# Optimization experiments

Measured on AMD Instinct MI355X. Metric: run time of the kernel, lower is better.

## Reference

```python
import jax, jax.numpy as jnp
import numpy as np
import math

B, N, D, K, H = 64, 16384, 64, 8, 128
ITERS = 3
LN_EPS = 1e-5  # torch LayerNorm default


def _ln(x, w, b):
    m = jnp.mean(x, axis=-1, keepdims=True)
    v = jnp.mean((x - m) ** 2, axis=-1, keepdims=True)
    return (x - m) * jax.lax.rsqrt(v + LN_EPS) * w + b


def setup_inputs() -> dict:
    key = jax.random.key(0)
    ks = jax.random.split(key, 20)
    s = 1.0 / math.sqrt(D)
    inp = {
        "inputs": jax.random.normal(ks[0], (B, N, D), jnp.float32),
        "noise": jax.random.normal(ks[1], (B, K, D), jnp.float32),
        "slots_mu": jax.random.normal(ks[2], (1, 1, D), jnp.float32),
        "slots_sigma": jax.random.uniform(ks[3], (1, 1, D), jnp.float32, -s, s),
        "ln_in_w": jnp.ones((D,), jnp.float32), "ln_in_b": jnp.zeros((D,), jnp.float32),
        "ln_slots_w": jnp.ones((D,), jnp.float32), "ln_slots_b": jnp.zeros((D,), jnp.float32),
        "ln_ff_w": jnp.ones((D,), jnp.float32), "ln_ff_b": jnp.zeros((D,), jnp.float32),
        "wk": jax.random.uniform(ks[4], (D, D), jnp.float32, -s, s),
        "bk": jax.random.uniform(ks[5], (D,), jnp.float32, -s, s),
        "wq": jax.random.uniform(ks[6], (D, D), jnp.float32, -s, s),
        "bq": jax.random.uniform(ks[7], (D,), jnp.float32, -s, s),
        "wv": jax.random.uniform(ks[8], (D, D), jnp.float32, -s, s),
        "bv": jax.random.uniform(ks[9], (D,), jnp.float32, -s, s),
        "gru_wih": jax.random.uniform(ks[10], (D, 3 * D), jnp.float32, -s, s),
        "gru_bih": jax.random.uniform(ks[11], (3 * D,), jnp.float32, -s, s),
        "gru_whh": jax.random.uniform(ks[12], (D, 3 * D), jnp.float32, -s, s),
        "gru_bhh": jax.random.uniform(ks[13], (3 * D,), jnp.float32, -s, s),
        "mlp_w1": jax.random.uniform(ks[14], (D, H), jnp.float32, -s, s),
        "mlp_b1": jax.random.uniform(ks[15], (H,), jnp.float32, -s, s),
        "mlp_w2": jax.random.uniform(ks[16], (H, D), jnp.float32, -1.0 / math.sqrt(H), 1.0 / math.sqrt(H)),
        "mlp_b2": jax.random.uniform(ks[17], (D,), jnp.float32, -1.0 / math.sqrt(H), 1.0 / math.sqrt(H)),
    }
    return inp


def reference(inputs, noise, slots_mu, slots_sigma, ln_in_w, ln_in_b,
              ln_slots_w, ln_slots_b, ln_ff_w, ln_ff_b,
              wk, bk, wq, bq, wv, bv,
              gru_wih, gru_bih, gru_whh, gru_bhh,
              mlp_w1, mlp_b1, mlp_w2, mlp_b2):
    x = _ln(inputs, ln_in_w, ln_in_b)              # [B, N, D]
    # k, v depend only on (fixed) inputs; original recomputes them each iter
    # with identical values, so hoist for efficiency (same math).
    k = x @ wk + bk                                 # [B, N, D]
    v = x @ wv + bv                                 # [B, N, D]
    slots = slots_mu + slots_sigma * noise          # [B, K, D]
    scale = 1.0 / math.sqrt(D)
    for _ in range(ITERS):
        prev = slots
        q = _ln(slots, ln_slots_w, ln_slots_b) @ wq + bq          # [B, K, D]
        logits = jnp.einsum('bkd,bnd->bkn', q, k) * scale          # [B, K, N]
        attn = jax.nn.softmax(logits, axis=1)  # softmax over slots
        updates = jnp.einsum('bkn,bnd->bkd', attn, v)              # [B, K, D]
        # torch GRUCell: gates ordered (r, z, n)
        gi = updates @ gru_wih + gru_bih                           # [B, K, 3D]
        gh = prev @ gru_whh + gru_bhh
        i_r, i_z, i_n = jnp.split(gi, 3, axis=-1)
        h_r, h_z, h_n = jnp.split(gh, 3, axis=-1)
        r = jax.nn.sigmoid(i_r + h_r)
        z = jax.nn.sigmoid(i_z + h_z)
        n = jnp.tanh(i_n + r * h_n)
        slots = (1.0 - z) * n + z * prev
        h = _ln(slots, ln_ff_w, ln_ff_b)
        slots = slots + (jax.nn.relu(h @ mlp_w1 + mlp_b1) @ mlp_w2 + mlp_b2)
    return slots
```

## Files before the change

kernel.cpp:

```cpp
#include <hip/hip_runtime.h>
#include <math.h>

#define B_ 64
#define N_ 16384
#define D_ 64
#define K_ 8
#define SCALE 0.125f
#define LN_EPS 1e-5f
#define CHUNKS 8
#define ROWS_PER_CHUNK (N_ / CHUNKS)
#define TILES (ROWS_PER_CHUNK / 256)
#define REC 528

__device__ __forceinline__ float wsum64(float v) {
#pragma unroll
  for (int m = 1; m < 64; m <<= 1) v += __shfl_xor(v, m);
  return v;
}

__global__ void init_slots(const float* __restrict__ noise, const float* __restrict__ mu,
                           const float* __restrict__ sg, float* __restrict__ slots) {
  int i = blockIdx.x * blockDim.x + threadIdx.x;
  int d = i & 63;
  slots[i] = mu[d] + sg[d] * noise[i];
}

__global__ __launch_bounds__(64) void prep_q(
    const float* __restrict__ slots,
    const float* __restrict__ lnsw, const float* __restrict__ lnsb,
    const float* __restrict__ wq, const float* __restrict__ bq,
    const float* __restrict__ wk, const float* __restrict__ bk,
    const float* __restrict__ lniw, const float* __restrict__ lnib,
    float* __restrict__ qprep) {
  const int bk_i = blockIdx.x;
  const int b = bk_i >> 3, kk = bk_i & 7;
  const int d = threadIdx.x;
  __shared__ float xs[64], qsh[64], wkl[64 * 65];
  for (int i = 0; i < 64; ++i) wkl[i * 65 + d] = wk[i * 64 + d];
  float s = slots[bk_i * 64 + d];
  float m = wsum64(s) * (1.f / 64.f);
  float df = s - m;
  float var = wsum64(df * df) * (1.f / 64.f);
  float r = 1.f / sqrtf(var + LN_EPS);
  xs[d] = df * r * lnsw[d] + lnsb[d];
  __syncthreads();
  float q = bq[d];
  for (int c = 0; c < 64; ++c) q += xs[c] * wq[c * 64 + d];
  qsh[d] = q;
  __syncthreads();
  float qp = 0.f, c0 = 0.f;
  for (int dd = 0; dd < 64; ++dd) {
    float qd = qsh[dd];
    qp += wkl[d * 65 + dd] * qd;
    c0 += qd * bk[dd];
  }
  float qw = qp * lniw[d] * SCALE;
  float As = wsum64(qw);
  float Bp = wsum64(qp * lnib[d]);
  float Bc = (Bp + c0) * SCALE;
  float* rec = qprep + b * REC;
  rec[d * 8 + kk] = qw;
  if (d == 0) { rec[512 + kk] = As; rec[520 + kk] = Bc; }
}

__global__ __launch_bounds__(256, 2) void attn_pass(
    const float* __restrict__ inp, const float* __restrict__ qprep,
    float* __restrict__ part) {
  __shared__ __align__(16) float xrow[256 * 68];
  __shared__ float2 aw[4 * 257];
  __shared__ float redST[64];
  const int tid = threadIdx.x;
  const int b = blockIdx.x >> 3, chunk = blockIdx.x & 7;
  const int p = tid & 3, dq = (tid >> 2) & 15, w = tid >> 6;
  const float* __restrict__ qp = qprep + b * REC;
  const float* srcbase = inp + ((size_t)b * N_ + (size_t)chunk * ROWS_PER_CHUNK) * D_;
  float4 x[16];
  {
    const float4* s = reinterpret_cast<const float4*>(srcbase + (size_t)tid * D_);
#pragma unroll
    for (int j = 0; j < 16; ++j) x[j] = s[j];
  }
  float Ya[8] = {0.f, 0.f, 0.f, 0.f, 0.f, 0.f, 0.f, 0.f};
  float sS[8] = {0.f, 0.f, 0.f, 0.f, 0.f, 0.f, 0.f, 0.f};
  float sT[8] = {0.f, 0.f, 0.f, 0.f, 0.f, 0.f, 0.f, 0.f};
  for (int t = 0; t < TILES; ++t) {
    float sum = 0.f, sq = 0.f;
    float l[8] = {0.f, 0.f, 0.f, 0.f, 0.f, 0.f, 0.f, 0.f};
#pragma unroll
    for (int j = 0; j < 16; ++j) {
      float xc[4] = {x[j].x, x[j].y, x[j].z, x[j].w};
#pragma unroll
      for (int e = 0; e < 4; ++e) {
        const int c = j * 4 + e;
        const float v = xc[e];
        sum += v; sq += v * v;
#pragma unroll
        for (int kq = 0; kq < 8; ++kq) l[kq] += qp[c * 8 + kq] * v;
      }
    }
    const float m = sum * (1.f / 64.f);
    const float var = sq * (1.f / 64.f) - m * m;
    const float r = 1.f / sqrtf(var + LN_EPS);
    const float mr = m * r;
    float lmax = -1e30f;
#pragma unroll
    for (int kq = 0; kq < 8; ++kq) {
      l[kq] = r * l[kq] - mr * qp[512 + kq] + qp[520 + kq];
      lmax = fmaxf(lmax, l[kq]);
    }
    float es = 0.f;
#pragma unroll
    for (int kq = 0; kq < 8; ++kq) { l[kq] = __expf(l[kq] - lmax); es += l[kq]; }
    const float inv = 1.f / es;
#pragma unroll
    for (int kq = 0; kq < 8; ++kq) {
      l[kq] *= inv;
      sS[kq] += l[kq];
      sT[kq] += l[kq] * mr;
    }
#pragma unroll
    for (int pp = 0; pp < 4; ++pp) {
      float2 v2; v2.x = l[2 * pp] * r; v2.y = l[2 * pp + 1] * r;
      aw[pp * 257 + tid] = v2;
    }
    {
      float* dst = &xrow[tid * 68];
      const int rs = tid >> 3;
#pragma unroll
      for (int j = 0; j < 16; ++j) {
        const int cs = (j + rs) & 15;
        *reinterpret_cast<float4*>(dst + cs * 4) = x[j];
      }
    }
    if (t + 1 < TILES) {
      const float4* s = reinterpret_cast<const float4*>(srcbase + (size_t)((t + 1) * 256 + tid) * D_);
#pragma unroll
      for (int j = 0; j < 16; ++j) x[j] = s[j];
    }
    __syncthreads();
#pragma unroll 4
    for (int i = 0; i < 64; ++i) {
      const int nl = w * 64 + i;
      const float2 a2 = aw[p * 257 + nl];
      const float4 xv = *reinterpret_cast<const float4*>(
          &xrow[nl * 68 + (((dq + (nl >> 3)) & 15) << 2)]);
      Ya[0] += a2.x * xv.x; Ya[1] += a2.x * xv.y; Ya[2] += a2.x * xv.z; Ya[3] += a2.x * xv.w;
      Ya[4] += a2.y * xv.x; Ya[5] += a2.y * xv.y; Ya[6] += a2.y * xv.z; Ya[7] += a2.y * xv.w;
    }
    __syncthreads();
  }
#pragma unroll
  for (int kq = 0; kq < 8; ++kq) { sS[kq] = wsum64(sS[kq]); sT[kq] = wsum64(sT[kq]); }
  if ((tid & 63) == 0) {
#pragma unroll
    for (int i = 0; i < 8; ++i) { redST[w * 16 + i] = sS[i]; redST[w * 16 + 8 + i] = sT[i]; }
  }
  float* yred = xrow;
  *reinterpret_cast<float4*>(&yred[tid * 12]) = make_float4(Ya[0], Ya[1], Ya[2], Ya[3]);
  *reinterpret_cast<float4*>(&yred[tid * 12 + 4]) = make_float4(Ya[4], Ya[5], Ya[6], Ya[7]);
  __syncthreads();
  float* dst = part + (size_t)blockIdx.x * REC;
  for (int o = tid; o < 512; o += 256) {
    const int kq = o >> 6, dd = o & 63;
    const int pp = kq >> 1, kkl = kq & 1, dqq = dd >> 2, jj = dd & 3;
    float v = 0.f;
#pragma unroll
    for (int ww = 0; ww < 4; ++ww)
      v += yred[(ww * 64 + dqq * 4 + pp) * 12 + kkl * 4 + jj];
    dst[o] = v;
  }
  if (tid < 16)
    dst[512 + tid] = redST[tid] + redST[16 + tid] + redST[32 + tid] + redST[48 + tid];
}

__global__ __launch_bounds__(256) void slot_update(
    const float* __restrict__ part, const float* slots_in,
    const float* __restrict__ lniw, const float* __restrict__ lnib,
    const float* __restrict__ wv, const float* __restrict__ bv,
    const float* __restrict__ wih, const float* __restrict__ bih,
    const float* __restrict__ whh, const float* __restrict__ bhh,
    const float* __restrict__ lnfw, const float* __restrict__ lnfb,
    const float* __restrict__ w1, const float* __restrict__ b1,
    const float* __restrict__ w2, const float* __restrict__ b2,
    const float* __restrict__ lnsw, const float* __restrict__ lnsb,
    const float* __restrict__ wq, const float* __restrict__ bq,
    const float* __restrict__ wk, const float* __restrict__ bkv,
    float* slots_out, float* __restrict__ qprep, const int do_prep) {
  const int bk_i = blockIdx.x, b = bk_i >> 3, kk = bk_i & 7;
  const int tid = threadIdx.x, cq = tid >> 6, d = tid & 63;
  const int c0 = cq * 16;
  __shared__ float pA[4][68], pB[4][68], pC[4][68], pD[4][68];
  __shared__ float xsh[64], psh[64], ush[64], hsh[64], snsh[64], qsh[64];
  __shared__ float hid1[2][132];
  const float* pb = part + (size_t)(b * CHUNKS) * REC;
  float S = 0.f, T1 = 0.f;
#pragma unroll
  for (int ch = 0; ch < CHUNKS; ++ch) {
    S += pb[ch * REC + 512 + kk];
    T1 += pb[ch * REC + 520 + kk];
  }
  float y = 0.f;
#pragma unroll
  for (int cc = 0; cc < 2; ++cc)
    y += pb[(cq * 2 + cc) * REC + kk * 64 + d];
  pA[cq][d] = y;
  const float prev = slots_in[bk_i * 64 + d];
  if (cq == 0) psh[d] = prev;
  __syncthreads();
  if (cq == 0) {
    const float Y = pA[0][d] + pA[1][d] + pA[2][d] + pA[3][d];
    xsh[d] = lniw[d] * (Y - T1) + lnib[d] * S;
  }
  __syncthreads();
  {
    float up = 0.f, h0 = 0.f, h1 = 0.f, h2 = 0.f;
    for (int c = c0; c < c0 + 16; ++c) {
      const float xc = xsh[c], pc = psh[c];
      up += wv[c * 64 + d] * xc;
      h0 += pc * whh[c * 192 + d];
      h1 += pc * whh[c * 192 + 64 + d];
      h2 += pc * whh[c * 192 + 128 + d];
    }
    pA[cq][d] = up; pB[cq][d] = h0; pC[cq][d] = h1; pD[cq][d] = h2;
  }
  __syncthreads();
  float hh0 = 0.f, hh1 = 0.f, hh2 = 0.f;
  if (cq == 0) {
    ush[d] = S * bv[d] + pA[0][d] + pA[1][d] + pA[2][d] + pA[3][d];
    hh0 = bhh[d] + pB[0][d] + pB[1][d] + pB[2][d] + pB[3][d];
    hh1 = bhh[64 + d] + pC[0][d] + pC[1][d] + pC[2][d] + pC[3][d];
    hh2 = bhh[128 + d] + pD[0][d] + pD[1][d] + pD[2][d] + pD[3][d];
  }
  __syncthreads();
  {
    float g0 = 0.f, g1 = 0.f, g2 = 0.f;
    for (int c = c0; c < c0 + 16; ++c) {
      const float uc = ush[c];
      g0 += uc * wih[c * 192 + d];
      g1 += uc * wih[c * 192 + 64 + d];
      g2 += uc * wih[c * 192 + 128 + d];
    }
    pA[cq][d] = g0; pB[cq][d] = g1; pC[cq][d] = g2;
  }
  __syncthreads();
  if (cq == 0) {
    const float gi0 = bih[d] + pA[0][d] + pA[1][d] + pA[2][d] + pA[3][d];
    const float gi1 = bih[64 + d] + pB[0][d] + pB[1][d] + pB[2][d] + pB[3][d];
    const float gi2 = bih[128 + d] + pC[0][d] + pC[1][d] + pC[2][d] + pC[3][d];
    const float rg = 1.f / (1.f + __expf(-(gi0 + hh0)));
    const float zg = 1.f / (1.f + __expf(-(gi1 + hh1)));
    const float ng = tanhf(gi2 + rg * hh2);
    const float sn = (1.f - zg) * ng + zg * prev;
    const float mm = wsum64(sn) * (1.f / 64.f);
    const float df = sn - mm;
    const float vv = wsum64(df * df) * (1.f / 64.f);
    const float rr = 1.f / sqrtf(vv + LN_EPS);
    snsh[d] = sn;
    hsh[d] = df * rr * lnfw[d] + lnfb[d];
  }
  __syncthreads();
  {
    const int j = tid & 127, ch2 = tid >> 7;
    float a = 0.f;
    for (int c = ch2 * 32; c < ch2 * 32 + 32; ++c) a += hsh[c] * w1[c * 128 + j];
    hid1[ch2][j] = a;
  }
  __syncthreads();
  {
    float o = 0.f;
    for (int j2 = cq * 32; j2 < cq * 32 + 32; ++j2) {
      const float hv = fmaxf(hid1[0][j2] + hid1[1][j2] + b1[j2], 0.f);
      o += hv * w2[j2 * 64 + d];
    }
    pA[cq][d] = o;
  }
  __syncthreads();
  float news = 0.f;
  if (cq == 0) {
    news = snsh[d] + b2[d] + pA[0][d] + pA[1][d] + pA[2][d] + pA[3][d];
    slots_out[bk_i * 64 + d] = news;
  }
  if (!do_prep) return;
  if (cq == 0) {
    const float mm = wsum64(news) * (1.f / 64.f);
    const float df = news - mm;
    const float vv = wsum64(df * df) * (1.f / 64.f);
    const float rr = 1.f / sqrtf(vv + LN_EPS);
    xsh[d] = df * rr * lnsw[d] + lnsb[d];
  }
  __syncthreads();
  {
    float qpt = 0.f;
    for (int c = c0; c < c0 + 16; ++c) qpt += xsh[c] * wq[c * 64 + d];
    pB[cq][d] = qpt;
  }
  __syncthreads();
  if (cq == 0) qsh[d] = bq[d] + pB[0][d] + pB[1][d] + pB[2][d] + pB[3][d];
  __syncthreads();
  {
    float qq = 0.f;
    for (int dd2 = c0; dd2 < c0 + 16; ++dd2) qq += wk[d * 64 + dd2] * qsh[dd2];
    pC[cq][d] = qq;
  }
  __syncthreads();
  if (cq == 0) {
    const float qpv = pC[0][d] + pC[1][d] + pC[2][d] + pC[3][d];
    const float c0v = wsum64(qsh[d] * bkv[d]);
    const float qw = qpv * lniw[d] * SCALE;
    const float As = wsum64(qw);
    const float Bp = wsum64(qpv * lnib[d]);
    const float Bc = (Bp + c0v) * SCALE;
    float* rec = qprep + b * REC;
    rec[d * 8 + kk] = qw;
    if (d == 0) { rec[512 + kk] = As; rec[520 + kk] = Bc; }
  }
}

extern "C" void kernel_launch(void* const* d_in, const int* in_sizes, int n_in,
                              void* d_out, int out_size, void* d_ws, size_t ws_size,
                              hipStream_t stream) {
  const float* inp   = (const float*)d_in[0];
  const float* noise = (const float*)d_in[1];
  const float* mu    = (const float*)d_in[2];
  const float* sg    = (const float*)d_in[3];
  const float* lniw  = (const float*)d_in[4];
  const float* lnib  = (const float*)d_in[5];
  const float* lnsw  = (const float*)d_in[6];
  const float* lnsb  = (const float*)d_in[7];
  const float* lnfw  = (const float*)d_in[8];
  const float* lnfb  = (const float*)d_in[9];
  const float* wk    = (const float*)d_in[10];
  const float* bk    = (const float*)d_in[11];
  const float* wq    = (const float*)d_in[12];
  const float* bq    = (const float*)d_in[13];
  const float* wv    = (const float*)d_in[14];
  const float* bv    = (const float*)d_in[15];
  const float* wih   = (const float*)d_in[16];
  const float* bih   = (const float*)d_in[17];
  const float* whh   = (const float*)d_in[18];
  const float* bhh   = (const float*)d_in[19];
  const float* w1    = (const float*)d_in[20];
  const float* b1    = (const float*)d_in[21];
  const float* w2    = (const float*)d_in[22];
  const float* b2    = (const float*)d_in[23];
  float* ws = (float*)d_ws;
  float* slots = ws;
  float* qprep = ws + 32768;
  float* part  = ws + 32768 + 64 * REC;
  float* out   = (float*)d_out;
  init_slots<<<64, 512, 0, stream>>>(noise, mu, sg, slots);
  prep_q<<<B_ * K_, 64, 0, stream>>>(slots, lnsw, lnsb, wq, bq, wk, bk, lniw, lnib, qprep);
  for (int it = 0; it < 3; ++it) {
    attn_pass<<<B_ * CHUNKS, 256, 0, stream>>>(inp, qprep, part);
    slot_update<<<B_ * K_, 256, 0, stream>>>(
        part, slots, lniw, lnib, wv, bv, wih, bih, whh, bhh,
        lnfw, lnfb, w1, b1, w2, b2, lnsw, lnsb, wq, bq, wk, bk,
        (it == 2) ? out : slots, qprep, (it < 2) ? 1 : 0);
  }
}
```

Baseline: 376.2 us.

## Double-buffer attention input tiles via direct global-to-LDS DMA loads

Restructures attn_pass to stream input tiles straight into shared memory with global_load_lds into a double buffer, so the next tile's fetch overlaps compute on the current one. Blocks grow to 512 threads over fewer chunks, with two threads splitting each row's logit dot products and combining them by shuffle. Query weights are staged in LDS for vector reads. This is meant to cut register pressure and global load latency stalls, at the cost of hand-placed waitcnt and barrier synchronisation that must be exactly right. The S/T partial sums are halved because both threads of a pair add them.

Measured after the change: 318.4 us. 15.4% less time.

```diff
diff --git a/kernel.cpp b/kernel.cpp
--- a/kernel.cpp
+++ b/kernel.cpp
@@ -3,19 +3,25 @@
 
 #define B_ 64
 #define N_ 16384
-#define D_ 64
 #define K_ 8
 #define SCALE 0.125f
 #define LN_EPS 1e-5f
-#define CHUNKS 8
+#define CHUNKS 4
 #define ROWS_PER_CHUNK (N_ / CHUNKS)
-#define TILES (ROWS_PER_CHUNK / 256)
+#define TILE 256
+#define TILES (ROWS_PER_CHUNK / TILE)
 #define REC 528
 
 __device__ __forceinline__ float wsum64(float v) {
 #pragma unroll
   for (int m = 1; m < 64; m <<= 1) v += __shfl_xor(v, m);
   return v;
+}
+
+__device__ __forceinline__ void dma16(const float* g, float* l) {
+  __builtin_amdgcn_global_load_lds(
+      (const __attribute__((address_space(1))) float*)g,
+      (__attribute__((address_space(3))) float*)l, 16, 0, 0);
 }
 
 __global__ void init_slots(const float* __restrict__ noise, const float* __restrict__ mu,
@@ -63,41 +69,85 @@
   if (d == 0) { rec[512 + kk] = As; rec[520 + kk] = Bc; }
 }
 
-__global__ __launch_bounds__(256, 2) void attn_pass(
+__global__ __launch_bounds__(512, 2) void attn_pass(
     const float* __restrict__ inp, const float* __restrict__ qprep,
     float* __restrict__ part) {
-  __shared__ __align__(16) float xrow[256 * 68];
-  __shared__ float2 aw[4 * 257];
-  __shared__ float redST[64];
+  __shared__ __align__(16) float xbuf[2][TILE * 64];
+  __shared__ __align__(16) float qwT[512];
+  __shared__ float2 aw[4][TILE + 4];
+  __shared__ float redST[128];
   const int tid = threadIdx.x;
-  const int b = blockIdx.x >> 3, chunk = blockIdx.x & 7;
-  const int p = tid & 3, dq = (tid >> 2) & 15, w = tid >> 6;
+  const int b = blockIdx.x >> 2, chunk = blockIdx.x & 3;
+  const int w = tid >> 6;
   const float* __restrict__ qp = qprep + b * REC;
-  const float* srcbase = inp + ((size_t)b * N_ + (size_t)chunk * ROWS_PER_CHUNK) * D_;
-  float4 x[16];
-  {
-    const float4* s = reinterpret_cast<const float4*>(srcbase + (size_t)tid * D_);
-#pragma unroll
-    for (int j = 0; j < 16; ++j) x[j] = s[j];
-  }
-  float Ya[8] = {0.f, 0.f, 0.f, 0.f, 0.f, 0.f, 0.f, 0.f};
-  float sS[8] = {0.f, 0.f, 0.f, 0.f, 0.f, 0.f, 0.f, 0.f};
-  float sT[8] = {0.f, 0.f, 0.f, 0.f, 0.f, 0.f, 0.f, 0.f};
+  const float* srcbase = inp + ((size_t)b * N_ + (size_t)chunk * ROWS_PER_CHUNK) * 64;
+  qwT[tid] = qp[tid];
+  float As_[8], Bc_[8];
+#pragma unroll
+  for (int kq = 0; kq < 8; ++kq) { As_[kq] = qp[512 + kq]; Bc_[kq] = qp[520 + kq]; }
+  __syncthreads();
+  {
+    const float* tb = srcbase;
+    float* lb = &xbuf[0][0];
+#pragma unroll
+    for (int r8 = 0; r8 < 8; ++r8) {
+      const int R = r8 * 32 + (tid >> 4);
+      const int q = tid & 15;
+      const int lj = (q - R) & 15;
+      dma16(tb + R * 64 + lj * 4, lb + (r8 * 512 + (tid & ~63)) * 4);
+    }
+  }
+  const int h = tid & 1, R = tid >> 1;
+  const int p = (tid & 63) >> 4, dqv = tid & 15;
+  float Ya[8] = {0,0,0,0,0,0,0,0};
+  float sS[8] = {0,0,0,0,0,0,0,0};
+  float sT[8] = {0,0,0,0,0,0,0,0};
   for (int t = 0; t < TILES; ++t) {
+    const int cur = t & 1;
+    __builtin_amdgcn_s_barrier();
+    if (t + 1 < TILES) {
+      const float* tb = srcbase + (size_t)(t + 1) * TILE * 64;
+      float* lb = &xbuf[cur ^ 1][0];
+#pragma unroll
+      for (int r8 = 0; r8 < 8; ++r8) {
+        const int Rr = r8 * 32 + (tid >> 4);
+        const int q = tid & 15;
+        const int lj = (q - Rr) & 15;
+        dma16(tb + Rr * 64 + lj * 4, lb + (r8 * 512 + (tid & ~63)) * 4);
+      }
+      asm volatile("s_waitcnt vmcnt(8)" ::: "memory");
+    } else {
+      asm volatile("s_waitcnt vmcnt(0)" ::: "memory");
+    }
+    __builtin_amdgcn_sched_barrier(0);
+    __builtin_amdgcn_s_barrier();
+    const float* rowp = &xbuf[cur][R * 64];
+    float4 xq[8];
+#pragma unroll
+    for (int jj = 0; jj < 8; ++jj) {
+      const int qph = (h * 8 + jj + R) & 15;
+      xq[jj] = *reinterpret_cast<const float4*>(&rowp[qph * 4]);
+    }
     float sum = 0.f, sq = 0.f;
-    float l[8] = {0.f, 0.f, 0.f, 0.f, 0.f, 0.f, 0.f, 0.f};
-#pragma unroll
-    for (int j = 0; j < 16; ++j) {
-      float xc[4] = {x[j].x, x[j].y, x[j].z, x[j].w};
+    float l[8] = {0,0,0,0,0,0,0,0};
+#pragma unroll
+    for (int jj = 0; jj < 8; ++jj) {
+      float xc[4] = {xq[jj].x, xq[jj].y, xq[jj].z, xq[jj].w};
 #pragma unroll
       for (int e = 0; e < 4; ++e) {
-        const int c = j * 4 + e;
+        const int c = h * 32 + jj * 4 + e;
         const float v = xc[e];
         sum += v; sq += v * v;
-#pragma unroll
-        for (int kq = 0; kq < 8; ++kq) l[kq] += qp[c * 8 + kq] * v;
+        const float4 qa = *reinterpret_cast<const float4*>(&qwT[c * 8]);
+        const float4 qb = *reinterpret_cast<const float4*>(&qwT[c * 8 + 4]);
+        l[0] += qa.x * v; l[1] += qa.y * v; l[2] += qa.z * v; l[3] += qa.w * v;
+        l[4] += qb.x * v; l[5] += qb.y * v; l[6] += qb.z * v; l[7] += qb.w * v;
       }
     }
+#pragma unroll
+    for (int kq = 0; kq < 8; ++kq) l[kq] += __shfl_xor(l[kq], 1);
+    sum += __shfl_xor(sum, 1);
+    sq  += __shfl_xor(sq, 1);
     const float m = sum * (1.f / 64.f);
     const float var = sq * (1.f / 64.f) - m * m;
     const float r = 1.f / sqrtf(var + LN_EPS);
@@ -105,7 +155,7 @@
     float lmax = -1e30f;
 #pragma unroll
     for (int kq = 0; kq < 8; ++kq) {
-      l[kq] = r * l[kq] - mr * qp[512 + kq] + qp[520 + kq];
+      l[kq] = r * l[kq] - mr * As_[kq] + Bc_[kq];
       lmax = fmaxf(lmax, l[kq]);
     }
     float es = 0.f;
@@ -118,36 +168,24 @@
       sS[kq] += l[kq];
       sT[kq] += l[kq] * mr;
     }
-#pragma unroll
-    for (int pp = 0; pp < 4; ++pp) {
-      float2 v2; v2.x = l[2 * pp] * r; v2.y = l[2 * pp + 1] * r;
-      aw[pp * 257 + tid] = v2;
-    }
-    {
-      float* dst = &xrow[tid * 68];
-      const int rs = tid >> 3;
-#pragma unroll
-      for (int j = 0; j < 16; ++j) {
-        const int cs = (j + rs) & 15;
-        *reinterpret_cast<float4*>(dst + cs * 4) = x[j];
+    if (h == 0) {
+#pragma unroll
+      for (int pp = 0; pp < 4; ++pp) {
+        float2 v2; v2.x = l[2 * pp] * r; v2.y = l[2 * pp + 1] * r;
+        aw[pp][R] = v2;
       }
     }
-    if (t + 1 < TILES) {
-      const float4* s = reinterpret_cast<const float4*>(srcbase + (size_t)((t + 1) * 256 + tid) * D_);
-#pragma unroll
-      for (int j = 0; j < 16; ++j) x[j] = s[j];
-    }
-    __syncthreads();
-#pragma unroll 4
-    for (int i = 0; i < 64; ++i) {
-      const int nl = w * 64 + i;
-      const float2 a2 = aw[p * 257 + nl];
+    asm volatile("s_waitcnt lgkmcnt(0)" ::: "memory");
+    __builtin_amdgcn_s_barrier();
+#pragma unroll 8
+    for (int i = 0; i < 32; ++i) {
+      const int nl = w * 32 + i;
+      const float2 a2 = aw[p][nl];
       const float4 xv = *reinterpret_cast<const float4*>(
-          &xrow[nl * 68 + (((dq + (nl >> 3)) & 15) << 2)]);
+          &xbuf[cur][nl * 64 + (((dqv + nl) & 15) << 2)]);
       Ya[0] += a2.x * xv.x; Ya[1] += a2.x * xv.y; Ya[2] += a2.x * xv.z; Ya[3] += a2.x * xv.w;
       Ya[4] += a2.y * xv.x; Ya[5] += a2.y * xv.y; Ya[6] += a2.y * xv.z; Ya[7] += a2.y * xv.w;
     }
-    __syncthreads();
   }
 #pragma unroll
   for (int kq = 0; kq < 8; ++kq) { sS[kq] = wsum64(sS[kq]); sT[kq] = wsum64(sT[kq]); }
@@ -155,22 +193,24 @@
 #pragma unroll
     for (int i = 0; i < 8; ++i) { redST[w * 16 + i] = sS[i]; redST[w * 16 + 8 + i] = sT[i]; }
   }
-  float* yred = xrow;
-  *reinterpret_cast<float4*>(&yred[tid * 12]) = make_float4(Ya[0], Ya[1], Ya[2], Ya[3]);
-  *reinterpret_cast<float4*>(&yred[tid * 12 + 4]) = make_float4(Ya[4], Ya[5], Ya[6], Ya[7]);
-  __syncthreads();
+  float* yr = &xbuf[0][0];
+  *reinterpret_cast<float4*>(&yr[tid * 8])     = make_float4(Ya[0], Ya[1], Ya[2], Ya[3]);
+  *reinterpret_cast<float4*>(&yr[tid * 8 + 4]) = make_float4(Ya[4], Ya[5], Ya[6], Ya[7]);
+  asm volatile("s_waitcnt lgkmcnt(0)" ::: "memory");
+  __builtin_amdgcn_s_barrier();
   float* dst = part + (size_t)blockIdx.x * REC;
-  for (int o = tid; o < 512; o += 256) {
-    const int kq = o >> 6, dd = o & 63;
-    const int pp = kq >> 1, kkl = kq & 1, dqq = dd >> 2, jj = dd & 3;
+  {
+    const int kq = tid >> 6, dd = tid & 63;
+    const int pp = kq >> 1, cc = kq & 1, dqq = dd >> 2, ee = dd & 3;
     float v = 0.f;
 #pragma unroll
-    for (int ww = 0; ww < 4; ++ww)
-      v += yred[(ww * 64 + dqq * 4 + pp) * 12 + kkl * 4 + jj];
-    dst[o] = v;
+    for (int ww = 0; ww < 8; ++ww)
+      v += yr[(ww * 64 + pp * 16 + dqq) * 8 + cc * 4 + ee];
+    dst[tid] = v;
   }
   if (tid < 16)
-    dst[512 + tid] = redST[tid] + redST[16 + tid] + redST[32 + tid] + redST[48 + tid];
+    dst[512 + tid] = 0.5f * (redST[tid] + redST[16 + tid] + redST[32 + tid] + redST[48 + tid] +
+                             redST[64 + tid] + redST[80 + tid] + redST[96 + tid] + redST[112 + tid]);
 }
 
 __global__ __launch_bounds__(256) void slot_update(
@@ -199,11 +239,7 @@
     S += pb[ch * REC + 512 + kk];
     T1 += pb[ch * REC + 520 + kk];
   }
-  float y = 0.f;
-#pragma unroll
-  for (int cc = 0; cc < 2; ++cc)
-    y += pb[(cq * 2 + cc) * REC + kk * 64 + d];
-  pA[cq][d] = y;
+  pA[cq][d] = pb[cq * REC + kk * 64 + d];
   const float prev = slots_in[bk_i * 64 + d];
   if (cq == 0) psh[d] = prev;
   __syncthreads();
@@ -351,7 +387,7 @@
   init_slots<<<64, 512, 0, stream>>>(noise, mu, sg, slots);
   prep_q<<<B_ * K_, 64, 0, stream>>>(slots, lnsw, lnsb, wq, bq, wk, bk, lniw, lnib, qprep);
   for (int it = 0; it < 3; ++it) {
-    attn_pass<<<B_ * CHUNKS, 256, 0, stream>>>(inp, qprep, part);
+    attn_pass<<<B_ * CHUNKS, 512, 0, stream>>>(inp, qprep, part);
     slot_update<<<B_ * K_, 256, 0, stream>>>(
         part, slots, lniw, lnib, wv, bv, wih, bih, whh, bhh,
         lnfw, lnfb, w1, b1, w2, b2, lnsw, lnsb, wq, bq, wk, bk,
```

## Stream input tiles via async global-to-LDS double buffering in attention pass

Applied to the files above, without the earlier changes.

The attention kernel now loads input rows straight into a double-buffered LDS tile with global_load_lds instead of staging them through registers and writing them to shared memory. The next tile's transfer overlaps with compute on the current one, synchronised by explicit waitcnt counters and barriers. The weighted-sum loop is restructured so each thread accumulates all 8 slots for 4 columns across 16 rows. The chunk count per batch drops to 4, which halves the grid to 256 blocks and removes the register-heavy launch bound. The larger LDS footprint (about 143 KB) and the smaller grid lower occupancy and parallelism.

After: 414.5 us. 10.2% more time.

```diff
diff --git a/kernel.cpp b/kernel.cpp
--- a/kernel.cpp
+++ b/kernel.cpp
@@ -3,19 +3,26 @@
 
 #define B_ 64
 #define N_ 16384
-#define D_ 64
 #define K_ 8
 #define SCALE 0.125f
 #define LN_EPS 1e-5f
-#define CHUNKS 8
+#define CHUNKS 4
 #define ROWS_PER_CHUNK (N_ / CHUNKS)
-#define TILES (ROWS_PER_CHUNK / 256)
+#define TILE 256
+#define TILES (ROWS_PER_CHUNK / TILE)
+#define CHSTR 260
 #define REC 528
 
 __device__ __forceinline__ float wsum64(float v) {
 #pragma unroll
   for (int m = 1; m < 64; m <<= 1) v += __shfl_xor(v, m);
   return v;
+}
+
+__device__ __forceinline__ void dma16(const float* g, float* l) {
+  __builtin_amdgcn_global_load_lds(
+      (const __attribute__((address_space(1))) float*)g,
+      (__attribute__((address_space(3))) float*)l, 16, 0, 0);
 }
 
 __global__ void init_slots(const float* __restrict__ noise, const float* __restrict__ mu,
@@ -63,32 +70,61 @@
   if (d == 0) { rec[512 + kk] = As; rec[520 + kk] = Bc; }
 }
 
-__global__ __launch_bounds__(256, 2) void attn_pass(
+__global__ __launch_bounds__(256) void attn_pass(
     const float* __restrict__ inp, const float* __restrict__ qprep,
     float* __restrict__ part) {
-  __shared__ __align__(16) float xrow[256 * 68];
-  __shared__ float2 aw[4 * 257];
+  __shared__ __align__(16) float xbuf[2][64 * CHSTR];
+  __shared__ __align__(16) float awb[256 * 10];
   __shared__ float redST[64];
   const int tid = threadIdx.x;
-  const int b = blockIdx.x >> 3, chunk = blockIdx.x & 7;
-  const int p = tid & 3, dq = (tid >> 2) & 15, w = tid >> 6;
+  const int w = tid >> 6, lane = tid & 63;
+  const int b = blockIdx.x >> 2, chunk4 = blockIdx.x & 3;
   const float* __restrict__ qp = qprep + b * REC;
-  const float* srcbase = inp + ((size_t)b * N_ + (size_t)chunk * ROWS_PER_CHUNK) * D_;
-  float4 x[16];
-  {
-    const float4* s = reinterpret_cast<const float4*>(srcbase + (size_t)tid * D_);
-#pragma unroll
-    for (int j = 0; j < 16; ++j) x[j] = s[j];
-  }
-  float Ya[8] = {0.f, 0.f, 0.f, 0.f, 0.f, 0.f, 0.f, 0.f};
-  float sS[8] = {0.f, 0.f, 0.f, 0.f, 0.f, 0.f, 0.f, 0.f};
-  float sT[8] = {0.f, 0.f, 0.f, 0.f, 0.f, 0.f, 0.f, 0.f};
+  const float* srcbase = inp + ((size_t)b * N_ + (size_t)chunk4 * ROWS_PER_CHUNK) * 64;
+  float As_[8], Bc_[8];
+#pragma unroll
+  for (int kq = 0; kq < 8; ++kq) { As_[kq] = qp[512 + kq]; Bc_[kq] = qp[520 + kq]; }
+#pragma unroll
+  for (int i = 0; i < 16; ++i) {
+    const int ch = w * 16 + i;
+    dma16(srcbase + ch * 256 + lane * 4, &xbuf[0][ch * CHSTR]);
+  }
+  const int R = tid;
+  const int g = lane >> 4, q = lane & 15;
+  float Ya[8][4];
+  float sS[8], sT[8];
+#pragma unroll
+  for (int kq = 0; kq < 8; ++kq) {
+    sS[kq] = 0.f; sT[kq] = 0.f;
+#pragma unroll
+    for (int e = 0; e < 4; ++e) Ya[kq][e] = 0.f;
+  }
   for (int t = 0; t < TILES; ++t) {
+    const int cur = t & 1;
+    asm volatile("s_waitcnt lgkmcnt(0)" ::: "memory");
+    __builtin_amdgcn_s_barrier();
+    __builtin_amdgcn_sched_barrier(0);
+    if (t + 1 < TILES) {
+      const float* tb = srcbase + (size_t)(t + 1) * TILE * 64;
+      float* lb = &xbuf[cur ^ 1][0];
+#pragma unroll
+      for (int i = 0; i < 16; ++i) {
+        const int ch = w * 16 + i;
+        dma16(tb + ch * 256 + lane * 4, lb + ch * CHSTR);
+      }
+      asm volatile("s_waitcnt vmcnt(16)" ::: "memory");
+    } else {
+      asm volatile("s_waitcnt vmcnt(0)" ::: "memory");
+    }
+    __builtin_amdgcn_sched_barrier(0);
+    __builtin_amdgcn_s_barrier();
+    const float* rowp = &xbuf[cur][(R >> 2) * CHSTR + (R & 3) * 64];
     float sum = 0.f, sq = 0.f;
-    float l[8] = {0.f, 0.f, 0.f, 0.f, 0.f, 0.f, 0.f, 0.f};
+    float l[8] = {0, 0, 0, 0, 0, 0, 0, 0};
 #pragma unroll
     for (int j = 0; j < 16; ++j) {
-      float xc[4] = {x[j].x, x[j].y, x[j].z, x[j].w};
+      const float4 xv = *reinterpret_cast<const float4*>(rowp + j * 4);
+      const float xc[4] = {xv.x, xv.y, xv.z, xv.w};
 #pragma unroll
       for (int e = 0; e < 4; ++e) {
         const int c = j * 4 + e;
@@ -105,7 +141,7 @@
     float lmax = -1e30f;
 #pragma unroll
     for (int kq = 0; kq < 8; ++kq) {
-      l[kq] = r * l[kq] - mr * qp[512 + kq] + qp[520 + kq];
+      l[kq] = r * l[kq] - mr * As_[kq] + Bc_[kq];
       lmax = fmaxf(lmax, l[kq]);
     }
     float es = 0.f;
@@ -114,59 +150,52 @@
     const float inv = 1.f / es;
 #pragma unroll
     for (int kq = 0; kq < 8; ++kq) {
-      l[kq] *= inv;
-      sS[kq] += l[kq];
-      sT[kq] += l[kq] * mr;
-    }
-#pragma unroll
-    for (int pp = 0; pp < 4; ++pp) {
-      float2 v2; v2.x = l[2 * pp] * r; v2.y = l[2 * pp + 1] * r;
-      aw[pp * 257 + tid] = v2;
-    }
-    {
-      float* dst = &xrow[tid * 68];
-      const int rs = tid >> 3;
-#pragma unroll
-      for (int j = 0; j < 16; ++j) {
-        const int cs = (j + rs) & 15;
-        *reinterpret_cast<float4*>(dst + cs * 4) = x[j];
+      const float a = l[kq] * inv;
+      sS[kq] += a;
+      sT[kq] += a * mr;
+      l[kq] = a * r;
+    }
+    *reinterpret_cast<float4*>(&awb[R * 10])     = make_float4(l[0], l[1], l[2], l[3]);
+    *reinterpret_cast<float4*>(&awb[R * 10 + 4]) = make_float4(l[4], l[5], l[6], l[7]);
+    asm volatile("s_waitcnt lgkmcnt(0)" ::: "memory");
+    __builtin_amdgcn_s_barrier();
+#pragma unroll 4
+    for (int i = 0; i < 16; ++i) {
+      const int chb = w * 16 + i;
+      const float* ap = &awb[(chb * 4 + g) * 10];
+      const float4 a0 = *reinterpret_cast<const float4*>(ap);
+      const float4 a1 = *reinterpret_cast<const float4*>(ap + 4);
+      const float4 xv = *reinterpret_cast<const float4*>(
+          &xbuf[cur][chb * CHSTR + g * 64 + (q << 2)]);
+      const float xc[4] = {xv.x, xv.y, xv.z, xv.w};
+#pragma unroll
+      for (int e = 0; e < 4; ++e) {
+        Ya[0][e] += a0.x * xc[e]; Ya[1][e] += a0.y * xc[e];
+        Ya[2][e] += a0.z * xc[e]; Ya[3][e] += a0.w * xc[e];
+        Ya[4][e] += a1.x * xc[e]; Ya[5][e] += a1.y * xc[e];
+        Ya[6][e] += a1.z * xc[e]; Ya[7][e] += a1.w * xc[e];
       }
     }
-    if (t + 1 < TILES) {
-      const float4* s = reinterpret_cast<const float4*>(srcbase + (size_t)((t + 1) * 256 + tid) * D_);
-#pragma unroll
-      for (int j = 0; j < 16; ++j) x[j] = s[j];
-    }
-    __syncthreads();
-#pragma unroll 4
-    for (int i = 0; i < 64; ++i) {
-      const int nl = w * 64 + i;
-      const float2 a2 = aw[p * 257 + nl];
-      const float4 xv = *reinterpret_cast<const float4*>(
-          &xrow[nl * 68 + (((dq + (nl >> 3)) & 15) << 2)]);
-      Ya[0] += a2.x * xv.x; Ya[1] += a2.x * xv.y; Ya[2] += a2.x * xv.z; Ya[3] += a2.x * xv.w;
-      Ya[4] += a2.y * xv.x; Ya[5] += a2.y * xv.y; Ya[6] += a2.y * xv.z; Ya[7] += a2.y * xv.w;
-    }
-    __syncthreads();
   }
 #pragma unroll
   for (int kq = 0; kq < 8; ++kq) { sS[kq] = wsum64(sS[kq]); sT[kq] = wsum64(sT[kq]); }
-  if ((tid & 63) == 0) {
+  if (lane == 0) {
 #pragma unroll
     for (int i = 0; i < 8; ++i) { redST[w * 16 + i] = sS[i]; redST[w * 16 + 8 + i] = sT[i]; }
   }
-  float* yred = xrow;
-  *reinterpret_cast<float4*>(&yred[tid * 12]) = make_float4(Ya[0], Ya[1], Ya[2], Ya[3]);
-  *reinterpret_cast<float4*>(&yred[tid * 12 + 4]) = make_float4(Ya[4], Ya[5], Ya[6], Ya[7]);
+  float* yr = &xbuf[0][0];
+#pragma unroll
+  for (int kq = 0; kq < 8; ++kq)
+    *reinterpret_cast<float4*>(yr + tid * 36 + kq * 4) =
+        make_float4(Ya[kq][0], Ya[kq][1], Ya[kq][2], Ya[kq][3]);
   __syncthreads();
   float* dst = part + (size_t)blockIdx.x * REC;
   for (int o = tid; o < 512; o += 256) {
-    const int kq = o >> 6, dd = o & 63;
-    const int pp = kq >> 1, kkl = kq & 1, dqq = dd >> 2, jj = dd & 3;
+    const int kq = o >> 6, col = o & 63;
+    const int qq = col >> 2, ee = col & 3;
     float v = 0.f;
 #pragma unroll
-    for (int ww = 0; ww < 4; ++ww)
-      v += yred[(ww * 64 + dqq * 4 + pp) * 12 + kkl * 4 + jj];
+    for (int s = 0; s < 16; ++s) v += yr[(s * 16 + qq) * 36 + kq * 4 + ee];
     dst[o] = v;
   }
   if (tid < 16)
@@ -199,11 +228,7 @@
     S += pb[ch * REC + 512 + kk];
     T1 += pb[ch * REC + 520 + kk];
   }
-  float y = 0.f;
-#pragma unroll
-  for (int cc = 0; cc < 2; ++cc)
-    y += pb[(cq * 2 + cc) * REC + kk * 64 + d];
-  pA[cq][d] = y;
+  pA[cq][d] = pb[cq * REC + kk * 64 + d];
   const float prev = slots_in[bk_i * 64 + d];
   if (cq == 0) psh[d] = prev;
   __syncthreads();
```

## Restructure attention pass into per-wave fp16 LDS tiles with more chunks

Applied to the files above, without the earlier changes.

The attention pass now gives each wave its own 64-row tile, staged in LDS as packed fp16 pairs together with fp16 attention weights. This removes the block-wide __syncthreads between the logit and accumulation phases and halves LDS footprint so four blocks fit per CU. The chunk count doubles to 16 per batch, and slot_update sums the extra partials. Storing x and attention weights in fp16 adds rounding error in the updates accumulation, and the register prefetch of the next tile is dropped.

Measured after the change: 319.3 us. 15.1% less time.

```diff
diff --git a/kernel.cpp b/kernel.cpp
--- a/kernel.cpp
+++ b/kernel.cpp
@@ -3,19 +3,28 @@
 
 #define B_ 64
 #define N_ 16384
-#define D_ 64
 #define K_ 8
 #define SCALE 0.125f
 #define LN_EPS 1e-5f
-#define CHUNKS 8
-#define ROWS_PER_CHUNK (N_ / CHUNKS)
-#define TILES (ROWS_PER_CHUNK / 256)
+#define CHUNKS 16
 #define REC 528
+
+typedef unsigned int u32;
+typedef __fp16 half2_t __attribute__((ext_vector_type(2)));
 
 __device__ __forceinline__ float wsum64(float v) {
 #pragma unroll
   for (int m = 1; m < 64; m <<= 1) v += __shfl_xor(v, m);
   return v;
+}
+
+__device__ __forceinline__ u32 pk16(float a, float b) {
+  half2_t h = __builtin_amdgcn_cvt_pkrtz(a, b);
+  return __builtin_bit_cast(u32, h);
+}
+__device__ __forceinline__ float2 up16(u32 u) {
+  half2_t h = __builtin_bit_cast(half2_t, u);
+  return make_float2((float)h.x, (float)h.y);
 }
 
 __global__ void init_slots(const float* __restrict__ noise, const float* __restrict__ mu,
@@ -63,32 +72,35 @@
   if (d == 0) { rec[512 + kk] = As; rec[520 + kk] = Bc; }
 }
 
-__global__ __launch_bounds__(256, 2) void attn_pass(
+__global__ __launch_bounds__(256, 4) void attn_pass(
     const float* __restrict__ inp, const float* __restrict__ qprep,
     float* __restrict__ part) {
-  __shared__ __align__(16) float xrow[256 * 68];
-  __shared__ float2 aw[4 * 257];
+  __shared__ u32 xls[4][64 * 34];
+  __shared__ u32 awl[4][64 * 5];
   __shared__ float redST[64];
   const int tid = threadIdx.x;
-  const int b = blockIdx.x >> 3, chunk = blockIdx.x & 7;
-  const int p = tid & 3, dq = (tid >> 2) & 15, w = tid >> 6;
+  const int w = tid >> 6, lane = tid & 63;
+  const int b = blockIdx.x >> 4, chunk = blockIdx.x & 15;
   const float* __restrict__ qp = qprep + b * REC;
-  const float* srcbase = inp + ((size_t)b * N_ + (size_t)chunk * ROWS_PER_CHUNK) * D_;
-  float4 x[16];
-  {
-    const float4* s = reinterpret_cast<const float4*>(srcbase + (size_t)tid * D_);
-#pragma unroll
-    for (int j = 0; j < 16; ++j) x[j] = s[j];
-  }
-  float Ya[8] = {0.f, 0.f, 0.f, 0.f, 0.f, 0.f, 0.f, 0.f};
-  float sS[8] = {0.f, 0.f, 0.f, 0.f, 0.f, 0.f, 0.f, 0.f};
-  float sT[8] = {0.f, 0.f, 0.f, 0.f, 0.f, 0.f, 0.f, 0.f};
-  for (int t = 0; t < TILES; ++t) {
+  const float* srcw = inp + ((size_t)b * N_ + (size_t)(chunk * 1024 + w * 256)) * 64;
+  float As_[8], Bc_[8];
+#pragma unroll
+  for (int kq = 0; kq < 8; ++kq) { As_[kq] = qp[512 + kq]; Bc_[kq] = qp[520 + kq]; }
+  u32* __restrict__ xw = xls[w];
+  u32* __restrict__ aww = awl[w];
+  const int rh = lane >> 5, kh = (lane >> 3) & 3, c8 = lane & 7;
+  float Y0[8] = {0, 0, 0, 0, 0, 0, 0, 0};
+  float Y1[8] = {0, 0, 0, 0, 0, 0, 0, 0};
+  float sS[8] = {0, 0, 0, 0, 0, 0, 0, 0};
+  float sT[8] = {0, 0, 0, 0, 0, 0, 0, 0};
+  for (int mt = 0; mt < 4; ++mt) {
+    const float4* src = reinterpret_cast<const float4*>(srcw + (size_t)(mt * 64 + lane) * 64);
     float sum = 0.f, sq = 0.f;
-    float l[8] = {0.f, 0.f, 0.f, 0.f, 0.f, 0.f, 0.f, 0.f};
+    float l[8] = {0, 0, 0, 0, 0, 0, 0, 0};
 #pragma unroll
     for (int j = 0; j < 16; ++j) {
-      float xc[4] = {x[j].x, x[j].y, x[j].z, x[j].w};
+      const float4 xv = src[j];
+      const float xc[4] = {xv.x, xv.y, xv.z, xv.w};
 #pragma unroll
       for (int e = 0; e < 4; ++e) {
         const int c = j * 4 + e;
@@ -97,6 +109,8 @@
 #pragma unroll
         for (int kq = 0; kq < 8; ++kq) l[kq] += qp[c * 8 + kq] * v;
       }
+      *reinterpret_cast<uint2*>(&xw[lane * 34 + j * 2]) =
+          make_uint2(pk16(xv.x, xv.y), pk16(xv.z, xv.w));
     }
     const float m = sum * (1.f / 64.f);
     const float var = sq * (1.f / 64.f) - m * m;
@@ -105,7 +119,7 @@
     float lmax = -1e30f;
 #pragma unroll
     for (int kq = 0; kq < 8; ++kq) {
-      l[kq] = r * l[kq] - mr * qp[512 + kq] + qp[520 + kq];
+      l[kq] = r * l[kq] - mr * As_[kq] + Bc_[kq];
       lmax = fmaxf(lmax, l[kq]);
     }
     float es = 0.f;
@@ -114,59 +128,54 @@
     const float inv = 1.f / es;
 #pragma unroll
     for (int kq = 0; kq < 8; ++kq) {
-      l[kq] *= inv;
-      sS[kq] += l[kq];
-      sT[kq] += l[kq] * mr;
-    }
-#pragma unroll
-    for (int pp = 0; pp < 4; ++pp) {
-      float2 v2; v2.x = l[2 * pp] * r; v2.y = l[2 * pp + 1] * r;
-      aw[pp * 257 + tid] = v2;
-    }
-    {
-      float* dst = &xrow[tid * 68];
-      const int rs = tid >> 3;
-#pragma unroll
-      for (int j = 0; j < 16; ++j) {
-        const int cs = (j + rs) & 15;
-        *reinterpret_cast<float4*>(dst + cs * 4) = x[j];
+      const float a = l[kq] * inv;
+      sS[kq] += a;
+      sT[kq] += a * mr;
+      l[kq] = a * r;
+    }
+#pragma unroll
+    for (int kh2 = 0; kh2 < 4; ++kh2)
+      aww[lane * 5 + kh2] = pk16(l[2 * kh2], l[2 * kh2 + 1]);
+#pragma unroll 4
+    for (int i = 0; i < 32; ++i) {
+      const int row = rh * 32 + i;
+      const float2 ap = up16(aww[row * 5 + kh]);
+      const uint2 q0 = *reinterpret_cast<const uint2*>(&xw[row * 34 + c8 * 4]);
+      const uint2 q1 = *reinterpret_cast<const uint2*>(&xw[row * 34 + c8 * 4 + 2]);
+      const u32 uu[4] = {q0.x, q0.y, q1.x, q1.y};
+#pragma unroll
+      for (int t = 0; t < 4; ++t) {
+        const float2 xp = up16(uu[t]);
+        Y0[2 * t]     += ap.x * xp.x;  Y0[2 * t + 1] += ap.x * xp.y;
+        Y1[2 * t]     += ap.y * xp.x;  Y1[2 * t + 1] += ap.y * xp.y;
       }
     }
-    if (t + 1 < TILES) {
-      const float4* s = reinterpret_cast<const float4*>(srcbase + (size_t)((t + 1) * 256 + tid) * D_);
-#pragma unroll
-      for (int j = 0; j < 16; ++j) x[j] = s[j];
-    }
-    __syncthreads();
-#pragma unroll 4
-    for (int i = 0; i < 64; ++i) {
-      const int nl = w * 64 + i;
-      const float2 a2 = aw[p * 257 + nl];
-      const float4 xv = *reinterpret_cast<const float4*>(
-          &xrow[nl * 68 + (((dq + (nl >> 3)) & 15) << 2)]);
-      Ya[0] += a2.x * xv.x; Ya[1] += a2.x * xv.y; Ya[2] += a2.x * xv.z; Ya[3] += a2.x * xv.w;
-      Ya[4] += a2.y * xv.x; Ya[5] += a2.y * xv.y; Ya[6] += a2.y * xv.z; Ya[7] += a2.y * xv.w;
-    }
-    __syncthreads();
   }
 #pragma unroll
   for (int kq = 0; kq < 8; ++kq) { sS[kq] = wsum64(sS[kq]); sT[kq] = wsum64(sT[kq]); }
-  if ((tid & 63) == 0) {
+  if (lane == 0) {
 #pragma unroll
     for (int i = 0; i < 8; ++i) { redST[w * 16 + i] = sS[i]; redST[w * 16 + 8 + i] = sT[i]; }
   }
-  float* yred = xrow;
-  *reinterpret_cast<float4*>(&yred[tid * 12]) = make_float4(Ya[0], Ya[1], Ya[2], Ya[3]);
-  *reinterpret_cast<float4*>(&yred[tid * 12 + 4]) = make_float4(Ya[4], Ya[5], Ya[6], Ya[7]);
+#pragma unroll
+  for (int e = 0; e < 8; ++e) {
+    Y0[e] += __shfl_xor(Y0[e], 32);
+    Y1[e] += __shfl_xor(Y1[e], 32);
+  }
+  float* yr = reinterpret_cast<float*>(xw);
+  if (lane < 32) {
+#pragma unroll
+    for (int e = 0; e < 8; ++e) {
+      yr[(2 * kh + 0) * 64 + c8 * 8 + e] = Y0[e];
+      yr[(2 * kh + 1) * 64 + c8 * 8 + e] = Y1[e];
+    }
+  }
   __syncthreads();
   float* dst = part + (size_t)blockIdx.x * REC;
   for (int o = tid; o < 512; o += 256) {
-    const int kq = o >> 6, dd = o & 63;
-    const int pp = kq >> 1, kkl = kq & 1, dqq = dd >> 2, jj = dd & 3;
     float v = 0.f;
 #pragma unroll
-    for (int ww = 0; ww < 4; ++ww)
-      v += yred[(ww * 64 + dqq * 4 + pp) * 12 + kkl * 4 + jj];
+    for (int ww = 0; ww < 4; ++ww) v += reinterpret_cast<const float*>(xls[ww])[o];
     dst[o] = v;
   }
   if (tid < 16)
@@ -199,11 +208,13 @@
     S += pb[ch * REC + 512 + kk];
     T1 += pb[ch * REC + 520 + kk];
   }
-  float y = 0.f;
-#pragma unroll
-  for (int cc = 0; cc < 2; ++cc)
-    y += pb[(cq * 2 + cc) * REC + kk * 64 + d];
-  pA[cq][d] = y;
+  {
+    float y = 0.f;
+#pragma unroll
+    for (int cc = 0; cc < 4; ++cc)
+      y += pb[(size_t)(cq * 4 + cc) * REC + kk * 64 + d];
+    pA[cq][d] = y;
+  }
   const float prev = slots_in[bk_i * 64 + d];
   if (cq == 0) psh[d] = prev;
   __syncthreads();
```
